# Performance work log

Measured on AMD Instinct MI355X. Metric: run time of the kernel, lower is better.

Reference implementation:

```python
import jax, jax.numpy as jnp
import numpy as np

N_NODES = 100000
N_EDGES = 1600000
DIM = 128
NUM_HEADS = 8
HEAD_DIM = DIM // NUM_HEADS


def setup_inputs() -> dict:
    key = jax.random.key(0)
    k_x, k_src, k_dst, k_wqkv, k_bqkv, k_wout, k_bout = jax.random.split(key, 7)
    x = jax.random.normal(k_x, (N_NODES, DIM), dtype=jnp.float32)
    src = jax.random.randint(k_src, (N_EDGES,), 0, N_NODES, dtype=jnp.int32)
    dst = jax.random.randint(k_dst, (N_EDGES,), 0, N_NODES, dtype=jnp.int32)
    s = 1.0 / np.sqrt(DIM)
    Wqkv = jax.random.uniform(k_wqkv, (DIM, 3 * DIM), jnp.float32, -s, s)
    bqkv = jax.random.uniform(k_bqkv, (3 * DIM,), jnp.float32, -s, s)
    Wout = jax.random.uniform(k_wout, (DIM, DIM), jnp.float32, -s, s)
    bout = jax.random.uniform(k_bout, (DIM,), jnp.float32, -s, s)
    return {"x": x, "Wqkv": Wqkv, "bqkv": bqkv, "Wout": Wout, "bout": bout,
            "src": src, "dst": dst}


def reference(x, Wqkv, bqkv, Wout, bout, src, dst):
    n = x.shape[0]
    scale = 1.0 / np.sqrt(HEAD_DIM)
    # QKV projection -> [N, H, 3*hd], split exactly like torch .split on last dim
    qkv = (x @ Wqkv + bqkv).reshape(n, NUM_HEADS, 3 * HEAD_DIM)
    q = qkv[..., :HEAD_DIM]                       # queries  [N, H, hd]
    k = qkv[..., HEAD_DIM:2 * HEAD_DIM]           # keys     [N, H, hd]
    v = qkv[..., 2 * HEAD_DIM:]                   # values   [N, H, hd]
    # u_dot_v: per edge (u=src, v=dst): dot(keys[u], queries[v]) per head
    scores = jnp.einsum('ehd,ehd->eh', k[src], q[dst]) * scale  # [E, H]
    # edge_softmax over incoming edges of each dst node
    m = jax.ops.segment_max(scores, dst, num_segments=n)        # [N, H]
    p = jnp.exp(scores - m[dst])                                # [E, H]
    denom = jax.ops.segment_sum(p, dst, num_segments=n)         # [N, H]
    probs = p / denom[dst]                                      # [E, H]
    # u_mul_e_sum: scatter-sum of values[src] * probs into dst
    msgs = v[src] * probs[:, :, None]                            # [E, H, hd]
    agg = jax.ops.segment_sum(msgs, dst, num_segments=n)         # [N, H, hd]
    out = agg.reshape(n, DIM) @ Wout + bout
    return out
```

## Files before the change

kernel.cpp:

```cpp
#include <hip/hip_runtime.h>
#include <cstdint>
#include <cstddef>

#define N_DIM 128
#define QKV_DIM 384
#define NUM_HEADS 8
#define HEAD_DIM 16
#define SCAN_B 256
#define SCAN_V 4
#define SCAN_TILE (SCAN_B * SCAN_V)

typedef unsigned int uint;
typedef unsigned short ushort;
typedef __attribute__((ext_vector_type(8))) short short8;
typedef __attribute__((ext_vector_type(4))) float f32x4;

__device__ __forceinline__ ushort f2bf(float f) {
    uint u = __float_as_uint(f);
    uint r = u + 0x7fffu + ((u >> 16) & 1u);
    return (ushort)(r >> 16);
}
__device__ __forceinline__ float bf_lo(uint u) { return __uint_as_float(u << 16); }
__device__ __forceinline__ float bf_hi(uint u) { return __uint_as_float(u & 0xffff0000u); }

__global__ void cvt_x_kernel(const float* __restrict__ x, uint* __restrict__ xb, long total4) {
    long i = (long)blockIdx.x * blockDim.x + threadIdx.x;
    if (i >= total4) return;
    float4 f = ((const float4*)x)[i];
    uint lo = (uint)f2bf(f.x) | ((uint)f2bf(f.y) << 16);
    uint hi = (uint)f2bf(f.z) | ((uint)f2bf(f.w) << 16);
    ((uint2*)xb)[i] = make_uint2(lo, hi);
}

__global__ void pack_w_kernel(const float* __restrict__ W, ushort* __restrict__ Wp, int N) {
    int idx = blockIdx.x * blockDim.x + threadIdx.x;
    if (idx >= 128 * N) return;
    int j = idx & 7;
    int l = (idx >> 3) & 63;
    int fs = idx >> 9;
    int T = fs >> 2, s = fs & 3;
    int k = s * 32 + (l >> 4) * 8 + j;
    int c = T * 16 + (l & 15);
    Wp[idx] = f2bf(W[k * N + c]);
}

__global__ __launch_bounds__(256) void qkv_gemm(const uint* __restrict__ xb,
                                                const ushort* __restrict__ Wp,
                                                const float* __restrict__ bqkv,
                                                float* __restrict__ qtab,
                                                ushort* __restrict__ kvb, int n) {
    int w = threadIdx.x >> 6, lane = threadIdx.x & 63;
    int node0 = blockIdx.x * 64 + w * 16;
    int m = lane & 15, quad = lane >> 4;
    int arow = node0 + m; if (arow >= n) arow = n - 1;
    const uint* xr = xb + (size_t)arow * 64;
    short8 A[4];
    #pragma unroll
    for (int s = 0; s < 4; ++s) {
        uint4 u = *(const uint4*)(xr + s * 16 + quad * 4);
        A[s] = *(short8*)&u;
    }
    for (int T = 0; T < 24; ++T) {
        f32x4 acc = {0.f, 0.f, 0.f, 0.f};
        const ushort* bp = Wp + ((size_t)(T * 4) * 64 + lane) * 8;
        #pragma unroll
        for (int s = 0; s < 4; ++s) {
            uint4 u = *(const uint4*)(bp + s * 512);
            short8 B = *(short8*)&u;
            acc = __builtin_amdgcn_mfma_f32_16x16x32_bf16(A[s], B, acc, 0, 0, 0);
        }
        int c = T * 16 + m;
        int hq = T / 3, wv = T % 3;
        float bb = bqkv[c];
        #pragma unroll
        for (int r = 0; r < 4; ++r) {
            int nd = node0 + quad * 4 + r;
            if (nd < n) {
                float v = acc[r] + bb;
                if (wv == 0) {
                    qtab[(size_t)nd * N_DIM + hq * 16 + m] = v;
                } else {
                    kvb[(size_t)nd * 256 + hq * 32 + (wv - 1) * 16 + m] = f2bf(v);
                }
            }
        }
    }
}

__global__ __launch_bounds__(256) void out_gemm(const uint* __restrict__ aggb,
                                                const ushort* __restrict__ Wp,
                                                const float* __restrict__ bout,
                                                float* __restrict__ out, int n) {
    int w = threadIdx.x >> 6, lane = threadIdx.x & 63;
    int node0 = blockIdx.x * 64 + w * 16;
    int m = lane & 15, quad = lane >> 4;
    int arow = node0 + m; if (arow >= n) arow = n - 1;
    const uint* ar = aggb + (size_t)arow * 64;
    short8 A[4];
    #pragma unroll
    for (int s = 0; s < 4; ++s) {
        uint4 u = *(const uint4*)(ar + s * 16 + quad * 4);
        A[s] = *(short8*)&u;
    }
    for (int T = 0; T < 8; ++T) {
        f32x4 acc = {0.f, 0.f, 0.f, 0.f};
        const ushort* bp = Wp + ((size_t)(T * 4) * 64 + lane) * 8;
        #pragma unroll
        for (int s = 0; s < 4; ++s) {
            uint4 u = *(const uint4*)(bp + s * 512);
            short8 B = *(short8*)&u;
            acc = __builtin_amdgcn_mfma_f32_16x16x32_bf16(A[s], B, acc, 0, 0, 0);
        }
        int c = T * 16 + m;
        float bb = bout[c];
        #pragma unroll
        for (int r = 0; r < 4; ++r) {
            int nd = node0 + quad * 4 + r;
            if (nd < n) out[(size_t)nd * N_DIM + c] = acc[r] + bb;
        }
    }
}

__global__ void hist_kernel(const int* __restrict__ dst, int* __restrict__ counts, int nE) {
    int e = blockIdx.x * blockDim.x + threadIdx.x;
    if (e < nE) atomicAdd(&counts[dst[e]], 1);
}

__global__ void scan1_kernel(const int* __restrict__ counts, int* __restrict__ offs,
                             int* __restrict__ partials, int n) {
    __shared__ int ts[SCAN_B];
    int t = threadIdx.x;
    int base = blockIdx.x * SCAN_TILE + t * SCAN_V;
    int v[SCAN_V];
    int s = 0;
    #pragma unroll
    for (int i = 0; i < SCAN_V; ++i) { v[i] = (base + i < n) ? counts[base + i] : 0; s += v[i]; }
    ts[t] = s;
    __syncthreads();
    for (int off = 1; off < SCAN_B; off <<= 1) {
        int x = (t >= off) ? ts[t - off] : 0;
        __syncthreads();
        ts[t] += x;
        __syncthreads();
    }
    int run = (t > 0) ? ts[t - 1] : 0;
    if (t == SCAN_B - 1) partials[blockIdx.x] = ts[SCAN_B - 1];
    #pragma unroll
    for (int i = 0; i < SCAN_V; ++i) { if (base + i < n) offs[base + i] = run; run += v[i]; }
}

__global__ void scan2_kernel(int* __restrict__ partials, int P) {
    __shared__ int ps[1024];
    int t = threadIdx.x;
    ps[t] = (t < P) ? partials[t] : 0;
    __syncthreads();
    for (int off = 1; off < 1024; off <<= 1) {
        int x = (t >= off) ? ps[t - off] : 0;
        __syncthreads();
        ps[t] += x;
        __syncthreads();
    }
    if (t < P) partials[t] = (t > 0) ? ps[t - 1] : 0;
}

__global__ void scan3_kernel(int* __restrict__ offs, const int* __restrict__ partials,
                             int* __restrict__ cursor, int n, int nE) {
    int i = blockIdx.x * blockDim.x + threadIdx.x;
    if (i < n) {
        int o = offs[i] + partials[i / SCAN_TILE];
        offs[i] = o;
        cursor[i] = o;
    }
    if (i == 0) offs[n] = nE;
}

__global__ __launch_bounds__(256) void scatter_src_shard(const int* __restrict__ src,
                                                         const int* __restrict__ dst,
                                                         int* __restrict__ cursor,
                                                         int* __restrict__ esrc,
                                                         int nE, int shardSize) {
    int shard = blockIdx.x & 7;
    int sub   = blockIdx.x >> 3;
    int nsub  = gridDim.x >> 3;
    int lo = shard * shardSize;
    int hi = lo + shardSize;
    int stride = nsub * blockDim.x;
    for (int e = sub * blockDim.x + threadIdx.x; e < nE; e += stride) {
        int d = dst[e];
        if (d >= lo && d < hi) {
            int pos = atomicAdd(&cursor[d], 1);
            esrc[pos] = src[e];
        }
    }
}

__global__ void attn_kernel(const float* __restrict__ qtab, const uint* __restrict__ kvu,
                            const int* __restrict__ esrc, const int* __restrict__ offs,
                            ushort* __restrict__ aggb, int n) {
    int node = blockIdx.x;
    int t = threadIdx.x;
    __shared__ float qs[16][8];
    __shared__ int   ss[16];
    __shared__ float pp[16][8];
    int h  = t >> 4, dd = t & 15;
    int h2 = t & 7,  el = t >> 3;
    {
        float qv = qtab[(size_t)node * N_DIM + t];
        qs[dd][h] = qv;
    }
    int start = offs[node];
    int deg = offs[node + 1] - start;
    float l = 0.f, acc = 0.f;
    __syncthreads();

    for (int c0 = 0; c0 < deg; c0 += 16) {
        int rem = deg - c0;
        int cn = rem < 16 ? rem : 16;
        if (t < 16) ss[t] = (t < cn) ? esrc[start + c0 + t] : 0;
        __syncthreads();
        float pv = 0.f;
        if (el < cn) {
            const uint* kr = kvu + (size_t)ss[el] * 128 + h2 * 16;
            uint4 A = *((const uint4*)kr);
            uint4 B = *((const uint4*)(kr + 4));
            float dot = 0.f;
            dot = fmaf(bf_lo(A.x), qs[0][h2],  dot); dot = fmaf(bf_hi(A.x), qs[1][h2],  dot);
            dot = fmaf(bf_lo(A.y), qs[2][h2],  dot); dot = fmaf(bf_hi(A.y), qs[3][h2],  dot);
            dot = fmaf(bf_lo(A.z), qs[4][h2],  dot); dot = fmaf(bf_hi(A.z), qs[5][h2],  dot);
            dot = fmaf(bf_lo(A.w), qs[6][h2],  dot); dot = fmaf(bf_hi(A.w), qs[7][h2],  dot);
            dot = fmaf(bf_lo(B.x), qs[8][h2],  dot); dot = fmaf(bf_hi(B.x), qs[9][h2],  dot);
            dot = fmaf(bf_lo(B.y), qs[10][h2], dot); dot = fmaf(bf_hi(B.y), qs[11][h2], dot);
            dot = fmaf(bf_lo(B.z), qs[12][h2], dot); dot = fmaf(bf_hi(B.z), qs[13][h2], dot);
            dot = fmaf(bf_lo(B.w), qs[14][h2], dot); dot = fmaf(bf_hi(B.w), qs[15][h2], dot);
            pv = __expf(dot * 0.25f);
        }
        pp[el][h2] = pv;
        __syncthreads();
        float psum = 0.f, vacc = 0.f;
        int voff = h * 16 + 8 + (dd >> 1);
        bool hi = (dd & 1);
        if (cn == 16) {
            uint vv[16];
            #pragma unroll
            for (int i = 0; i < 16; ++i) vv[i] = kvu[(size_t)ss[i] * 128 + voff];
            #pragma unroll
            for (int i = 0; i < 16; ++i) {
                float p = pp[i][h];
                float v = hi ? bf_hi(vv[i]) : bf_lo(vv[i]);
                vacc = fmaf(p, v, vacc);
                psum += p;
            }
        } else {
            for (int i = 0; i < cn; ++i) {
                float p = pp[i][h];
                uint u = kvu[(size_t)ss[i] * 128 + voff];
                float v = hi ? bf_hi(u) : bf_lo(u);
                vacc = fmaf(p, v, vacc);
                psum += p;
            }
        }
        l   += psum;
        acc += vacc;
        __syncthreads();
    }
    aggb[(size_t)node * N_DIM + t] = f2bf((l > 0.f) ? acc / l : 0.f);
}

extern "C" void kernel_launch(void* const* d_in, const int* in_sizes, int n_in,
                              void* d_out, int out_size, void* d_ws, size_t ws_size,
                              hipStream_t stream) {
    const float* x    = (const float*)d_in[0];
    const float* Wqkv = (const float*)d_in[1];
    const float* bqkv = (const float*)d_in[2];
    const float* Wout = (const float*)d_in[3];
    const float* bout = (const float*)d_in[4];
    const int*   src  = (const int*)d_in[5];
    const int*   dst  = (const int*)d_in[6];
    float* out = (float*)d_out;

    const int n  = in_sizes[0] / N_DIM;
    const int nE = in_sizes[5];

    uint* ws = (uint*)d_ws;
    float*  qtab   = (float*)ws;
    uint*   kvu    = ws + (size_t)n * 128;
    uint*   aggb   = kvu + (size_t)n * 128;
    uint*   xb     = aggb + (size_t)n * 64;
    ushort* WpQ    = (ushort*)(xb + (size_t)n * 64);
    ushort* WpO    = WpQ + 128 * QKV_DIM;
    int*    counts = (int*)(WpO + 128 * N_DIM);
    int*    offs   = counts + n;
    int*    cursor = offs + n + 1;
    int*    partials = cursor + n;
    int*    esrc   = partials + 1024;

    hipMemsetAsync(counts, 0, (size_t)n * sizeof(int), stream);

    long total4 = (long)n * 32;
    cvt_x_kernel<<<(int)((total4 + 255) / 256), 256, 0, stream>>>(x, xb, total4);
    pack_w_kernel<<<(128 * QKV_DIM + 255) / 256, 256, 0, stream>>>(Wqkv, WpQ, QKV_DIM);
    pack_w_kernel<<<(128 * N_DIM + 255) / 256, 256, 0, stream>>>(Wout, WpO, N_DIM);

    qkv_gemm<<<(n + 63) / 64, 256, 0, stream>>>(xb, WpQ, bqkv, qtab, (ushort*)kvu, n);

    hist_kernel<<<(nE + 255) / 256, 256, 0, stream>>>(dst, counts, nE);
    int P = (n + SCAN_TILE - 1) / SCAN_TILE;
    scan1_kernel<<<P, SCAN_B, 0, stream>>>(counts, offs, partials, n);
    scan2_kernel<<<1, 1024, 0, stream>>>(partials, P);
    scan3_kernel<<<(n + 255) / 256, 256, 0, stream>>>(offs, partials, cursor, n, nE);

    int shardSize = (n + 7) / 8;
    scatter_src_shard<<<8 * 128, 256, 0, stream>>>(src, dst, cursor, esrc, nE, shardSize);

    attn_kernel<<<n, 128, 0, stream>>>(qtab, kvu, esrc, offs, (ushort*)aggb, n);

    out_gemm<<<(n + 63) / 64, 256, 0, stream>>>(aggb, WpO, bout, out, n);
}
```

Baseline: 460.8 us.

## Fuse x bf16 conversion into QKV GEMM, merge weight packing, streamline attention indexing

New measurement: 470.2 us. 2.0% more time.

```diff
diff --git a/kernel.cpp b/kernel.cpp
--- a/kernel.cpp
+++ b/kernel.cpp
@@ -23,18 +23,19 @@
 __device__ __forceinline__ float bf_lo(uint u) { return __uint_as_float(u << 16); }
 __device__ __forceinline__ float bf_hi(uint u) { return __uint_as_float(u & 0xffff0000u); }
 
-__global__ void cvt_x_kernel(const float* __restrict__ x, uint* __restrict__ xb, long total4) {
-    long i = (long)blockIdx.x * blockDim.x + threadIdx.x;
-    if (i >= total4) return;
-    float4 f = ((const float4*)x)[i];
-    uint lo = (uint)f2bf(f.x) | ((uint)f2bf(f.y) << 16);
-    uint hi = (uint)f2bf(f.z) | ((uint)f2bf(f.w) << 16);
-    ((uint2*)xb)[i] = make_uint2(lo, hi);
-}
-
-__global__ void pack_w_kernel(const float* __restrict__ W, ushort* __restrict__ Wp, int N) {
+__global__ void pack_w_kernel(const float* __restrict__ Wq, const float* __restrict__ Wo,
+                              ushort* __restrict__ WpQ, ushort* __restrict__ WpO) {
     int idx = blockIdx.x * blockDim.x + threadIdx.x;
-    if (idx >= 128 * N) return;
+    const float* W;
+    ushort* Wp;
+    int N;
+    if (idx < 128 * QKV_DIM) {
+        W = Wq; Wp = WpQ; N = QKV_DIM;
+    } else {
+        idx -= 128 * QKV_DIM;
+        if (idx >= 128 * N_DIM) return;
+        W = Wo; Wp = WpO; N = N_DIM;
+    }
     int j = idx & 7;
     int l = (idx >> 3) & 63;
     int fs = idx >> 9;
@@ -44,7 +45,7 @@
     Wp[idx] = f2bf(W[k * N + c]);
 }
 
-__global__ __launch_bounds__(256) void qkv_gemm(const uint* __restrict__ xb,
+__global__ __launch_bounds__(256) void qkv_gemm(const float* __restrict__ x,
                                                 const ushort* __restrict__ Wp,
                                                 const float* __restrict__ bqkv,
                                                 float* __restrict__ qtab,
@@ -53,11 +54,17 @@
     int node0 = blockIdx.x * 64 + w * 16;
     int m = lane & 15, quad = lane >> 4;
     int arow = node0 + m; if (arow >= n) arow = n - 1;
-    const uint* xr = xb + (size_t)arow * 64;
+    const float* xr = x + (size_t)arow * N_DIM;
     short8 A[4];
     #pragma unroll
     for (int s = 0; s < 4; ++s) {
-        uint4 u = *(const uint4*)(xr + s * 16 + quad * 4);
+        float4 f0 = *(const float4*)(xr + s * 32 + quad * 8);
+        float4 f1 = *(const float4*)(xr + s * 32 + quad * 8 + 4);
+        uint u0 = (uint)f2bf(f0.x) | ((uint)f2bf(f0.y) << 16);
+        uint u1 = (uint)f2bf(f0.z) | ((uint)f2bf(f0.w) << 16);
+        uint u2 = (uint)f2bf(f1.x) | ((uint)f2bf(f1.y) << 16);
+        uint u3 = (uint)f2bf(f1.z) | ((uint)f2bf(f1.w) << 16);
+        uint4 u = make_uint4(u0, u1, u2, u3);
         A[s] = *(short8*)&u;
     }
     for (int T = 0; T < 24; ++T) {
@@ -200,8 +207,9 @@
     int node = blockIdx.x;
     int t = threadIdx.x;
     __shared__ float qs[16][8];
-    __shared__ int   ss[16];
+    __shared__ uint  so[16];
     __shared__ float pp[16][8];
+    __shared__ float lw[2][8];
     int h  = t >> 4, dd = t & 15;
     int h2 = t & 7,  el = t >> 3;
     {
@@ -210,17 +218,19 @@
     }
     int start = offs[node];
     int deg = offs[node + 1] - start;
-    float l = 0.f, acc = 0.f;
+    float lsum = 0.f, acc = 0.f;
+    int voff = h * 16 + 8 + (dd >> 1);
+    bool hi = (dd & 1);
     __syncthreads();
 
     for (int c0 = 0; c0 < deg; c0 += 16) {
         int rem = deg - c0;
         int cn = rem < 16 ? rem : 16;
-        if (t < 16) ss[t] = (t < cn) ? esrc[start + c0 + t] : 0;
+        if (t < 16) so[t] = (t < cn) ? ((uint)esrc[start + c0 + t] << 9) : 0u;
         __syncthreads();
         float pv = 0.f;
         if (el < cn) {
-            const uint* kr = kvu + (size_t)ss[el] * 128 + h2 * 16;
+            const uint* kr = (const uint*)((const char*)kvu + so[el]) + h2 * 16;
             uint4 A = *((const uint4*)kr);
             uint4 B = *((const uint4*)(kr + 4));
             float dot = 0.f;
@@ -235,34 +245,40 @@
             pv = __expf(dot * 0.25f);
         }
         pp[el][h2] = pv;
-        __syncthreads();
-        float psum = 0.f, vacc = 0.f;
-        int voff = h * 16 + 8 + (dd >> 1);
-        bool hi = (dd & 1);
+        lsum += pv;
+        __syncthreads();
+        float vacc = 0.f;
         if (cn == 16) {
             uint vv[16];
             #pragma unroll
-            for (int i = 0; i < 16; ++i) vv[i] = kvu[(size_t)ss[i] * 128 + voff];
+            for (int i = 0; i < 16; ++i) {
+                uint off = (uint)__builtin_amdgcn_readfirstlane((int)so[i]);
+                vv[i] = *((const uint*)((const char*)kvu + off) + voff);
+            }
             #pragma unroll
             for (int i = 0; i < 16; ++i) {
                 float p = pp[i][h];
                 float v = hi ? bf_hi(vv[i]) : bf_lo(vv[i]);
                 vacc = fmaf(p, v, vacc);
-                psum += p;
             }
         } else {
             for (int i = 0; i < cn; ++i) {
+                uint off = (uint)__builtin_amdgcn_readfirstlane((int)so[i]);
                 float p = pp[i][h];
-                uint u = kvu[(size_t)ss[i] * 128 + voff];
+                uint u = *((const uint*)((const char*)kvu + off) + voff);
                 float v = hi ? bf_hi(u) : bf_lo(u);
                 vacc = fmaf(p, v, vacc);
-                psum += p;
             }
         }
-        l   += psum;
         acc += vacc;
         __syncthreads();
     }
+    lsum += __shfl_xor(lsum, 8, 64);
+    lsum += __shfl_xor(lsum, 16, 64);
+    lsum += __shfl_xor(lsum, 32, 64);
+    if ((t & 63) < 8) lw[t >> 6][t & 7] = lsum;
+    __syncthreads();
+    float l = lw[0][h] + lw[1][h];
     aggb[(size_t)node * N_DIM + t] = f2bf((l > 0.f) ? acc / l : 0.f);
 }
 
@@ -285,8 +301,7 @@
     float*  qtab   = (float*)ws;
     uint*   kvu    = ws + (size_t)n * 128;
     uint*   aggb   = kvu + (size_t)n * 128;
-    uint*   xb     = aggb + (size_t)n * 64;
-    ushort* WpQ    = (ushort*)(xb + (size_t)n * 64);
+    ushort* WpQ    = (ushort*)(aggb + (size_t)n * 64);
     ushort* WpO    = WpQ + 128 * QKV_DIM;
     int*    counts = (int*)(WpO + 128 * N_DIM);
     int*    offs   = counts + n;
@@ -296,12 +311,9 @@
 
     hipMemsetAsync(counts, 0, (size_t)n * sizeof(int), stream);
 
-    long total4 = (long)n * 32;
-    cvt_x_kernel<<<(int)((total4 + 255) / 256), 256, 0, stream>>>(x, xb, total4);
-    pack_w_kernel<<<(128 * QKV_DIM + 255) / 256, 256, 0, stream>>>(Wqkv, WpQ, QKV_DIM);
-    pack_w_kernel<<<(128 * N_DIM + 255) / 256, 256, 0, stream>>>(Wout, WpO, N_DIM);
-
-    qkv_gemm<<<(n + 63) / 64, 256, 0, stream>>>(xb, WpQ, bqkv, qtab, (ushort*)kvu, n);
+    pack_w_kernel<<<(128 * (QKV_DIM + N_DIM) + 255) / 256, 256, 0, stream>>>(Wqkv, Wout, WpQ, WpO);
+
+    qkv_gemm<<<(n + 63) / 64, 256, 0, stream>>>(x, WpQ, bqkv, qtab, (ushort*)kvu, n);
 
     hist_kernel<<<(nE + 255) / 256, 256, 0, stream>>>(dst, counts, nE);
     int P = (n + SCAN_TILE - 1) / SCAN_TILE;
```
